# Optimization experiments

Hardware: AMD Instinct MI355X
Metric: run time of the kernel (lower is better)

## Reference

```python
import jax, jax.numpy as jnp
import numpy as np

VOCAB, VDIM, DDIM, BATCH = 50257, 300, 512, 16


def setup_inputs() -> dict:
    key = jax.random.key(0)
    k1, k2, k3, k4, k5 = jax.random.split(key, 5)
    return {
        "decoder_hidden": jax.random.normal(k1, (BATCH, DDIM), dtype=jnp.float32),
        "embedding_vocab": jax.random.normal(k2, (VOCAB, VDIM), dtype=jnp.float32),
        "W_dec": jax.random.normal(k3, (VDIM, DDIM), dtype=jnp.float32) * (1.0 / np.sqrt(DDIM)),
        "b_dec": jax.random.normal(k4, (VDIM,), dtype=jnp.float32) * 0.01,
        "W_full": jax.random.normal(k5, (VDIM,), dtype=jnp.float32) * (1.0 / np.sqrt(VDIM)),
        "b_full": jnp.zeros((), dtype=jnp.float32),
    }


def reference(decoder_hidden, embedding_vocab, W_dec, b_dec, W_full, b_full):
    # query: (B, vocab_dim) = decoder_att(decoder_hidden)
    query = decoder_hidden @ W_dec.T + b_dec
    # additive scores: relu(vocab + query) projected to scalar -> (B, V)
    hidden = jax.nn.relu(embedding_vocab[None, :, :] + query[:, None, :])  # (B, V, D)
    att = jnp.einsum("bvd,d->bv", hidden, W_full) + b_full
    alpha = jax.nn.softmax(att, axis=1)  # softmax over vocab
    # weighted sum of vocab embeddings: (B, vocab_dim)
    attention_weighted_encoding = jnp.einsum("bv,vd->bd", alpha, embedding_vocab)
    return attention_weighted_encoding, alpha
```

## Files before the change

### kernel.cpp

```cpp
#include <hip/hip_runtime.h>

constexpr int V  = 50257;
constexpr int D  = 300;
constexpr int KD = 512;
constexpr int B  = 16;

constexpr int ROWS = 32;
constexpr int NB_ATT = (V + ROWS - 1) / ROWS;
constexpr int NT = 5;
constexpr int NC  = 448;
constexpr int RPC = 113;

constexpr float NEG_HUGE = -1.0e30f;

constexpr size_t WS_QT   = 0;
constexpr size_t WS_STAT = 5120;
constexpr size_t WS_MS   = WS_STAT + (size_t)NB_ATT * 32;
constexpr size_t WS_PART = WS_MS + 32;
constexpr size_t WS_TMP  = WS_PART + (size_t)NC * 4800;

typedef float v2f __attribute__((ext_vector_type(2)));

struct f4 { float v[4]; };
__device__ __forceinline__ f4 ld4(const float* p) {
    float4 t = *(const float4*)p;
    return {t.x, t.y, t.z, t.w};
}

#define AS1 __attribute__((address_space(1)))
#define AS3 __attribute__((address_space(3)))
#define DPPF(x, CTRL) __int_as_float(__builtin_amdgcn_mov_dpp(__float_as_int(x), (CTRL), 0xF, 0xF, false))

__global__ void __launch_bounds__(256) k_query(
    const float* __restrict__ dh, const float* __restrict__ Wdec,
    const float* __restrict__ bdec, float* __restrict__ q_swz)
{
    int wid  = (blockIdx.x * 256 + threadIdx.x) >> 6;
    int lane = threadIdx.x & 63;
    if (wid >= 320 * 16) return;
    int d = wid >> 4, b = wid & 15;
    float s = 0.f;
    if (d < D) {
        const float* wrow = Wdec + (size_t)d * KD;
        const float* hrow = dh + (size_t)b * KD;
        for (int k = lane; k < KD; k += 64) s += wrow[k] * hrow[k];
        #pragma unroll
        for (int off = 32; off; off >>= 1) s += __shfl_down(s, off, 64);
        s += bdec[d];
    }
    if (lane == 0) {
        int P = (d >> 1) * 8 + ((((d & 1) << 2) | (b >> 2)) ^ ((d >> 2) & 7));
        q_swz[P * 4 + (b & 3)] = (d < D) ? s : 0.f;
    }
}

__global__ void __launch_bounds__(256) k_att(
    const float* __restrict__ E, const float* __restrict__ q_swz,
    const float* __restrict__ wf, const float* __restrict__ bf,
    float* __restrict__ att, float* __restrict__ blkstats)
{
    __shared__ __align__(16) float sq[5120];
    __shared__ __align__(16) float seE[9632];
    __shared__ float sms[768];

    const int t    = threadIdx.x;
    const int slot = t & 15;
    const int rg   = t >> 4;
    const int v0   = blockIdx.x * ROWS;

    #pragma unroll
    for (int k = 0; k < 5; ++k)
        __builtin_amdgcn_global_load_lds((const AS1 void*)(q_swz + k * 1024 + t * 4),
                                         (AS3 void*)(sq + k * 1024 + t * 4), 16, 0, 0);
    int nrow = V - v0; if (nrow > ROWS) nrow = ROWS;
    const int nflt = nrow * 300;
    const float* Eb = E + (size_t)v0 * 300;
    #pragma unroll
    for (int k = 0; k < 10; ++k) {
        int o = k * 1024 + t * 4;
        if (o < nflt)
            __builtin_amdgcn_global_load_lds((const AS1 void*)(Eb + o),
                                             (AS3 void*)(seE + o), 16, 0, 0);
    }
    if (t < 32) seE[9600 + t] = 0.f;

    f4 wreg[NT];
    #pragma unroll
    for (int k = 0; k < 4; ++k) wreg[k] = ld4(wf + k * 64 + slot * 4);
    if (slot < 11) wreg[4] = ld4(wf + 256 + slot * 4);
    else { wreg[4].v[0] = wreg[4].v[1] = wreg[4].v[2] = wreg[4].v[3] = 0.f; }
    #pragma unroll
    for (int i = 0; i < 4; ++i)
        if (256 + slot * 4 + i >= D && slot < 11) wreg[4].v[i] = 0.f;
    const float bfull = bf[0];

    int xq[2][4];
    #pragma unroll
    for (int i1 = 0; i1 < 2; ++i1)
        #pragma unroll
        for (int bq = 0; bq < 4; ++bq)
            xq[i1][bq] = slot * 64 + 4 * (((i1 << 2) | bq) ^ (slot & 7));

    v2f acc2[2][8];
    #pragma unroll
    for (int j = 0; j < 2; ++j)
        #pragma unroll
        for (int p = 0; p < 8; ++p) acc2[j][p] = (v2f){0.f, 0.f};

    __syncthreads();

    #pragma unroll
    for (int tt = 0; tt < NT; ++tt) {
        f4 e0 = ld4(seE + rg * 300 + tt * 64 + slot * 4);
        f4 e1 = ld4(seE + (rg + 16) * 300 + tt * 64 + slot * 4);
        const float* sqt = sq + tt * 1024;
        #pragma unroll
        for (int i = 0; i < 4; ++i) {
            float wi = wreg[tt].v[i];
            v2f w2 = {wi, wi};
            #pragma unroll
            for (int bq = 0; bq < 4; ++bq) {
                f4 qv = ld4(sqt + (i >> 1) * 32 + xq[i & 1][bq]);
                v2f qlo = {qv.v[0], qv.v[1]};
                v2f qhi = {qv.v[2], qv.v[3]};
                v2f z2  = {0.f, 0.f};
                v2f ea  = {e0.v[i], e0.v[i]};
                v2f lo0 = __builtin_elementwise_max(ea + qlo, z2);
                v2f hi0 = __builtin_elementwise_max(ea + qhi, z2);
                acc2[0][bq*2]   = __builtin_elementwise_fma(lo0, w2, acc2[0][bq*2]);
                acc2[0][bq*2+1] = __builtin_elementwise_fma(hi0, w2, acc2[0][bq*2+1]);
                v2f eb  = {e1.v[i], e1.v[i]};
                v2f lo1 = __builtin_elementwise_max(eb + qlo, z2);
                v2f hi1 = __builtin_elementwise_max(eb + qhi, z2);
                acc2[1][bq*2]   = __builtin_elementwise_fma(lo1, w2, acc2[1][bq*2]);
                acc2[1][bq*2+1] = __builtin_elementwise_fma(hi1, w2, acc2[1][bq*2+1]);
            }
        }
    }

    float acc[2][16];
    #pragma unroll
    for (int j = 0; j < 2; ++j)
        #pragma unroll
        for (int bq = 0; bq < 4; ++bq) {
            acc[j][bq*4+0] = acc2[j][bq*2][0];
            acc[j][bq*4+1] = acc2[j][bq*2][1];
            acc[j][bq*4+2] = acc2[j][bq*2+1][0];
            acc[j][bq*4+3] = acc2[j][bq*2+1][1];
        }

    #pragma unroll
    for (int j = 0; j < 2; ++j)
        #pragma unroll
        for (int b = 0; b < 16; ++b) {
            float x = acc[j][b];
            x += DPPF(x, 0xB1);
            x += DPPF(x, 0x4E);
            acc[j][b] = x;
        }
    const int c = slot & 3;
    float kept[2][4];
    #pragma unroll
    for (int j = 0; j < 2; ++j)
        #pragma unroll
        for (int kk = 0; kk < 4; ++kk) {
            float x = (c == 0) ? acc[j][kk]
                    : (c == 1) ? acc[j][4 + kk]
                    : (c == 2) ? acc[j][8 + kk]
                    :            acc[j][12 + kk];
            x += __shfl_xor(x, 4, 64);
            x += __shfl_xor(x, 8, 64);
            kept[j][kk] = x;
        }

    const int jown = (slot >> 2) & 1;
    const int dup  = slot >> 3;
    const int row  = v0 + rg + 16 * jown;
    const bool ok  = row < V;
    const int g    = rg + 16 * jown;
    #pragma unroll
    for (int kk2 = 0; kk2 < 2; ++kk2) {
        int b = 4 * c + (dup ? 2 : 0) + kk2;
        float x0 = jown ? kept[1][kk2]     : kept[0][kk2];
        float x1 = jown ? kept[1][2 + kk2] : kept[0][2 + kk2];
        float x  = (dup ? x1 : x0) + bfull;
        if (ok) att[(size_t)b * V + row] = x;
        sms[g * 16 + b] = ok ? x : NEG_HUGE;
    }
    __syncthreads();
    if (t < 128) {
        int b = t & 15, gq = t >> 4;
        float m = NEG_HUGE;
        #pragma unroll
        for (int u = 0; u < 4; ++u) m = fmaxf(m, sms[(gq * 4 + u) * 16 + b]);
        float s = 0.f;
        #pragma unroll
        for (int u = 0; u < 4; ++u) s += __expf(sms[(gq * 4 + u) * 16 + b] - m);
        sms[512 + gq * 16 + b] = m;
        sms[640 + gq * 16 + b] = s;
    }
    __syncthreads();
    if (t < 16) {
        float m = NEG_HUGE, s = 0.f;
        #pragma unroll
        for (int gq = 0; gq < 8; ++gq) {
            float mg = sms[512 + gq * 16 + t], sg = sms[640 + gq * 16 + t];
            float mn = fmaxf(m, mg);
            s = s * __expf(m - mn) + sg * __expf(mg - mn);
            m = mn;
        }
        blkstats[((size_t)blockIdx.x * 16 + t) * 2]     = m;
        blkstats[((size_t)blockIdx.x * 16 + t) * 2 + 1] = s;
    }
}

__global__ void __launch_bounds__(64) k_combine(
    const float* __restrict__ blkstats, float* __restrict__ MS)
{
    int b = blockIdx.x, lane = threadIdx.x;
    float m = NEG_HUGE;
    for (int cc = lane; cc < NB_ATT; cc += 64)
        m = fmaxf(m, blkstats[(size_t)(cc * 16 + b) * 2]);
    #pragma unroll
    for (int off = 32; off; off >>= 1) m = fmaxf(m, __shfl_xor(m, off, 64));
    float s = 0.f;
    for (int cc = lane; cc < NB_ATT; cc += 64)
        s += blkstats[(size_t)(cc * 16 + b) * 2 + 1] *
             __expf(blkstats[(size_t)(cc * 16 + b) * 2] - m);
    #pragma unroll
    for (int off = 32; off; off >>= 1) s += __shfl_xor(s, off, 64);
    if (lane == 0) { MS[b * 2] = m; MS[b * 2 + 1] = 1.f / s; }
}

__global__ void __launch_bounds__(320) k_awsum(
    const float* __restrict__ E, float* __restrict__ att,
    const float* __restrict__ MS, float* __restrict__ partials)
{
    __shared__ float sal[RPC * 16];
    int c = blockIdx.x, t = threadIdx.x;
    int v0 = c * RPC;
    int n = V - v0;
    if (n > RPC) n = RPC;
    if (n < 0) n = 0;

    for (int i = t; i < RPC * 16; i += 320) {
        int b = i / RPC, vv = i - b * RPC;
        float a = 0.f;
        if (vv < n) {
            float M = MS[b * 2], invS = MS[b * 2 + 1];
            size_t gi = (size_t)b * V + v0 + vv;
            a = __expf(att[gi] - M) * invS;
            att[gi] = a;
        }
        sal[vv * 16 + b] = a;
    }
    __syncthreads();

    if (t < D) {
        float acc[16];
        #pragma unroll
        for (int b = 0; b < 16; ++b) acc[b] = 0.f;
        #pragma unroll 8
        for (int vv = 0; vv < n; ++vv) {
            float e = E[(size_t)(v0 + vv) * D + t];
            const float* ap = sal + vv * 16;
            f4 a0 = ld4(ap), a1 = ld4(ap + 4), a2 = ld4(ap + 8), a3 = ld4(ap + 12);
            #pragma unroll
            for (int b = 0; b < 4; ++b) {
                acc[b]      = fmaf(a0.v[b], e, acc[b]);
                acc[b + 4]  = fmaf(a1.v[b], e, acc[b + 4]);
                acc[b + 8]  = fmaf(a2.v[b], e, acc[b + 8]);
                acc[b + 12] = fmaf(a3.v[b], e, acc[b + 12]);
            }
        }
        #pragma unroll
        for (int b = 0; b < 16; ++b)
            partials[(size_t)c * 4800 + b * D + t] = acc[b];
    }
}

__global__ void __launch_bounds__(256) k_red1(
    const float* __restrict__ partials, float* __restrict__ tmp)
{
    int o4 = blockIdx.x * 256 + threadIdx.x;
    if (o4 >= 1200) return;
    int y = blockIdx.y;
    float4 s = {0.f, 0.f, 0.f, 0.f};
    for (int c = y * 28; c < y * 28 + 28; ++c) {
        float4 p = *(const float4*)(partials + (size_t)c * 4800 + o4 * 4);
        s.x += p.x; s.y += p.y; s.z += p.z; s.w += p.w;
    }
    *(float4*)(tmp + (size_t)y * 4800 + o4 * 4) = s;
}

__global__ void __launch_bounds__(256) k_red2(
    const float* __restrict__ tmp, float* __restrict__ out)
{
    int o4 = blockIdx.x * 256 + threadIdx.x;
    if (o4 >= 1200) return;
    float4 s = {0.f, 0.f, 0.f, 0.f};
    #pragma unroll
    for (int y = 0; y < 16; ++y) {
        float4 p = *(const float4*)(tmp + (size_t)y * 4800 + o4 * 4);
        s.x += p.x; s.y += p.y; s.z += p.z; s.w += p.w;
    }
    *(float4*)(out + o4 * 4) = s;
}

extern "C" void kernel_launch(void* const* d_in, const int* in_sizes, int n_in,
                              void* d_out, int out_size, void* d_ws, size_t ws_size,
                              hipStream_t stream) {
    const float* dh   = (const float*)d_in[0];
    const float* E    = (const float*)d_in[1];
    const float* Wdec = (const float*)d_in[2];
    const float* bdec = (const float*)d_in[3];
    const float* wf   = (const float*)d_in[4];
    const float* bf   = (const float*)d_in[5];
    float* out = (float*)d_out;
    float* ws  = (float*)d_ws;

    float* q_swz = ws + WS_QT;
    float* stats = ws + WS_STAT;
    float* MS    = ws + WS_MS;
    float* part  = ws + WS_PART;
    float* tmp   = ws + WS_TMP;
    float* att   = out + 4800;

    k_query<<<(320 * 16) / 4, 256, 0, stream>>>(dh, Wdec, bdec, q_swz);
    k_att<<<NB_ATT, 256, 0, stream>>>(E, q_swz, wf, bf, att, stats);
    k_combine<<<B, 64, 0, stream>>>(stats, MS);
    k_awsum<<<NC, 320, 0, stream>>>(E, att, MS, part);
    k_red1<<<dim3(5, 16), 256, 0, stream>>>(part, tmp);
    k_red2<<<5, 256, 0, stream>>>(tmp, out);
}
```

Baseline: 74.37 us.

## Fuse attention scoring with online-softmax weighted sum over vocab tiles

```diff
diff --git a/kernel.cpp b/kernel.cpp
--- a/kernel.cpp
+++ b/kernel.cpp
@@ -5,19 +5,16 @@
 constexpr int KD = 512;
 constexpr int B  = 16;
 
-constexpr int ROWS = 32;
-constexpr int NB_ATT = (V + ROWS - 1) / ROWS;
-constexpr int NT = 5;
-constexpr int NC  = 448;
-constexpr int RPC = 113;
+constexpr int ROWS = 64;
+constexpr int NBLK = (V + ROWS - 1) / ROWS;
+constexpr int NSUB = NBLK * 2;
 
 constexpr float NEG_HUGE = -1.0e30f;
 
-constexpr size_t WS_QT   = 0;
-constexpr size_t WS_STAT = 5120;
-constexpr size_t WS_MS   = WS_STAT + (size_t)NB_ATT * 32;
-constexpr size_t WS_PART = WS_MS + 32;
-constexpr size_t WS_TMP  = WS_PART + (size_t)NC * 4800;
+constexpr size_t WS_QT    = 0;
+constexpr size_t WS_STAT  = 5120;
+constexpr size_t WS_SCALE = 55424;
+constexpr size_t WS_WPART = 80576;
 
 typedef float v2f __attribute__((ext_vector_type(2)));
 
@@ -54,14 +51,16 @@
     }
 }
 
-__global__ void __launch_bounds__(256) k_att(
+__global__ void __launch_bounds__(256, 2) k_att_pv(
     const float* __restrict__ E, const float* __restrict__ q_swz,
     const float* __restrict__ wf, const float* __restrict__ bf,
-    float* __restrict__ att, float* __restrict__ blkstats)
+    float* __restrict__ alpha, float* __restrict__ blkstats,
+    float* __restrict__ wpart)
 {
     __shared__ __align__(16) float sq[5120];
-    __shared__ __align__(16) float seE[9632];
-    __shared__ float sms[768];
+    __shared__ __align__(16) float seE[9600];
+    __shared__ float satt[512];
+    __shared__ float sm[16], sf[16], sold[16];
 
     const int t    = threadIdx.x;
     const int slot = t & 15;
@@ -72,19 +71,22 @@
     for (int k = 0; k < 5; ++k)
         __builtin_amdgcn_global_load_lds((const AS1 void*)(q_swz + k * 1024 + t * 4),
                                          (AS3 void*)(sq + k * 1024 + t * 4), 16, 0, 0);
-    int nrow = V - v0; if (nrow > ROWS) nrow = ROWS;
-    const int nflt = nrow * 300;
-    const float* Eb = E + (size_t)v0 * 300;
-    #pragma unroll
-    for (int k = 0; k < 10; ++k) {
-        int o = k * 1024 + t * 4;
-        if (o < nflt)
-            __builtin_amdgcn_global_load_lds((const AS1 void*)(Eb + o),
-                                             (AS3 void*)(seE + o), 16, 0, 0);
-    }
-    if (t < 32) seE[9600 + t] = 0.f;
-
-    f4 wreg[NT];
+    {
+        int nr = V - v0; if (nr > 32) nr = 32;
+        int nflt = nr * 300;
+        const float* Eb = E + (size_t)v0 * 300;
+        #pragma unroll
+        for (int k = 0; k < 10; ++k) {
+            int o = k * 1024 + t * 4;
+            if (o < nflt)
+                __builtin_amdgcn_global_load_lds((const AS1 void*)(Eb + o),
+                                                 (AS3 void*)(seE + o), 16, 0, 0);
+        }
+        for (int o = t * 4; o < 9600; o += 1024)
+            if (o >= nflt) *(float4*)(seE + o) = make_float4(0.f, 0.f, 0.f, 0.f);
+    }
+
+    f4 wreg[5];
     #pragma unroll
     for (int k = 0; k < 4; ++k) wreg[k] = ld4(wf + k * 64 + slot * 4);
     if (slot < 11) wreg[4] = ld4(wf + 256 + slot * 4);
@@ -101,210 +103,282 @@
         for (int bq = 0; bq < 4; ++bq)
             xq[i1][bq] = slot * 64 + 4 * (((i1 << 2) | bq) ^ (slot & 7));
 
-    v2f acc2[2][8];
-    #pragma unroll
-    for (int j = 0; j < 2; ++j)
-        #pragma unroll
-        for (int p = 0; p < 8; ++p) acc2[j][p] = (v2f){0.f, 0.f};
-
+    if (t < 16) sold[t] = NEG_HUGE;
+
+    const int dgrp = t & 15;
+    const int rh   = (t >> 4) & 1;
+    const int bp   = t >> 5;
+    const int b0   = bp * 2, b1 = bp * 2 + 1;
+    f4 pvA[5], pvB[5];
+    #pragma unroll
+    for (int k = 0; k < 5; ++k)
+        #pragma unroll
+        for (int c4 = 0; c4 < 4; ++c4) { pvA[k].v[c4] = 0.f; pvB[k].v[c4] = 0.f; }
+
+    asm volatile("s_waitcnt vmcnt(0)" ::: "memory");
     __syncthreads();
 
-    #pragma unroll
-    for (int tt = 0; tt < NT; ++tt) {
-        f4 e0 = ld4(seE + rg * 300 + tt * 64 + slot * 4);
-        f4 e1 = ld4(seE + (rg + 16) * 300 + tt * 64 + slot * 4);
-        const float* sqt = sq + tt * 1024;
-        #pragma unroll
-        for (int i = 0; i < 4; ++i) {
-            float wi = wreg[tt].v[i];
-            v2f w2 = {wi, wi};
-            #pragma unroll
-            for (int bq = 0; bq < 4; ++bq) {
-                f4 qv = ld4(sqt + (i >> 1) * 32 + xq[i & 1][bq]);
-                v2f qlo = {qv.v[0], qv.v[1]};
-                v2f qhi = {qv.v[2], qv.v[3]};
-                v2f z2  = {0.f, 0.f};
-                v2f ea  = {e0.v[i], e0.v[i]};
-                v2f lo0 = __builtin_elementwise_max(ea + qlo, z2);
-                v2f hi0 = __builtin_elementwise_max(ea + qhi, z2);
-                acc2[0][bq*2]   = __builtin_elementwise_fma(lo0, w2, acc2[0][bq*2]);
-                acc2[0][bq*2+1] = __builtin_elementwise_fma(hi0, w2, acc2[0][bq*2+1]);
-                v2f eb  = {e1.v[i], e1.v[i]};
-                v2f lo1 = __builtin_elementwise_max(eb + qlo, z2);
-                v2f hi1 = __builtin_elementwise_max(eb + qhi, z2);
-                acc2[1][bq*2]   = __builtin_elementwise_fma(lo1, w2, acc2[1][bq*2]);
-                acc2[1][bq*2+1] = __builtin_elementwise_fma(hi1, w2, acc2[1][bq*2+1]);
-            }
-        }
-    }
-
-    float acc[2][16];
-    #pragma unroll
-    for (int j = 0; j < 2; ++j)
-        #pragma unroll
-        for (int bq = 0; bq < 4; ++bq) {
-            acc[j][bq*4+0] = acc2[j][bq*2][0];
-            acc[j][bq*4+1] = acc2[j][bq*2][1];
-            acc[j][bq*4+2] = acc2[j][bq*2+1][0];
-            acc[j][bq*4+3] = acc2[j][bq*2+1][1];
-        }
-
-    #pragma unroll
-    for (int j = 0; j < 2; ++j)
-        #pragma unroll
-        for (int b = 0; b < 16; ++b) {
-            float x = acc[j][b];
-            x += DPPF(x, 0xB1);
-            x += DPPF(x, 0x4E);
-            acc[j][b] = x;
-        }
-    const int c = slot & 3;
-    float kept[2][4];
-    #pragma unroll
-    for (int j = 0; j < 2; ++j)
-        #pragma unroll
-        for (int kk = 0; kk < 4; ++kk) {
-            float x = (c == 0) ? acc[j][kk]
-                    : (c == 1) ? acc[j][4 + kk]
-                    : (c == 2) ? acc[j][8 + kk]
-                    :            acc[j][12 + kk];
-            x += __shfl_xor(x, 4, 64);
-            x += __shfl_xor(x, 8, 64);
-            kept[j][kk] = x;
-        }
-
+    const int c    = slot & 3;
     const int jown = (slot >> 2) & 1;
     const int dup  = slot >> 3;
-    const int row  = v0 + rg + 16 * jown;
-    const bool ok  = row < V;
-    const int g    = rg + 16 * jown;
-    #pragma unroll
-    for (int kk2 = 0; kk2 < 2; ++kk2) {
-        int b = 4 * c + (dup ? 2 : 0) + kk2;
-        float x0 = jown ? kept[1][kk2]     : kept[0][kk2];
-        float x1 = jown ? kept[1][2 + kk2] : kept[0][2 + kk2];
-        float x  = (dup ? x1 : x0) + bfull;
-        if (ok) att[(size_t)b * V + row] = x;
-        sms[g * 16 + b] = ok ? x : NEG_HUGE;
-    }
-    __syncthreads();
-    if (t < 128) {
-        int b = t & 15, gq = t >> 4;
-        float m = NEG_HUGE;
-        #pragma unroll
-        for (int u = 0; u < 4; ++u) m = fmaxf(m, sms[(gq * 4 + u) * 16 + b]);
-        float s = 0.f;
-        #pragma unroll
-        for (int u = 0; u < 4; ++u) s += __expf(sms[(gq * 4 + u) * 16 + b] - m);
-        sms[512 + gq * 16 + b] = m;
-        sms[640 + gq * 16 + b] = s;
-    }
-    __syncthreads();
-    if (t < 16) {
-        float m = NEG_HUGE, s = 0.f;
-        #pragma unroll
-        for (int gq = 0; gq < 8; ++gq) {
-            float mg = sms[512 + gq * 16 + t], sg = sms[640 + gq * 16 + t];
-            float mn = fmaxf(m, mg);
-            s = s * __expf(m - mn) + sg * __expf(mg - mn);
-            m = mn;
-        }
-        blkstats[((size_t)blockIdx.x * 16 + t) * 2]     = m;
-        blkstats[((size_t)blockIdx.x * 16 + t) * 2 + 1] = s;
+    const int lrow = rg + 16 * jown;
+
+    for (int sub = 0; sub < 2; ++sub) {
+        const int vs = v0 + sub * 32;
+
+        v2f acc2[2][8];
+        #pragma unroll
+        for (int j = 0; j < 2; ++j)
+            #pragma unroll
+            for (int p = 0; p < 8; ++p) acc2[j][p] = (v2f){0.f, 0.f};
+
+        #pragma unroll
+        for (int tt = 0; tt < 5; ++tt) {
+            f4 e0 = ld4(seE + rg * 300 + tt * 64 + slot * 4);
+            f4 e1 = ld4(seE + (rg + 16) * 300 + tt * 64 + slot * 4);
+            const float* sqt = sq + tt * 1024;
+            #pragma unroll
+            for (int i = 0; i < 4; ++i) {
+                float wi = wreg[tt].v[i];
+                v2f w2 = {wi, wi};
+                #pragma unroll
+                for (int bq = 0; bq < 4; ++bq) {
+                    f4 qv = ld4(sqt + (i >> 1) * 32 + xq[i & 1][bq]);
+                    v2f qlo = {qv.v[0], qv.v[1]};
+                    v2f qhi = {qv.v[2], qv.v[3]};
+                    v2f z2  = {0.f, 0.f};
+                    v2f ea  = {e0.v[i], e0.v[i]};
+                    v2f lo0 = __builtin_elementwise_max(ea + qlo, z2);
+                    v2f hi0 = __builtin_elementwise_max(ea + qhi, z2);
+                    acc2[0][bq*2]   = __builtin_elementwise_fma(lo0, w2, acc2[0][bq*2]);
+                    acc2[0][bq*2+1] = __builtin_elementwise_fma(hi0, w2, acc2[0][bq*2+1]);
+                    v2f eb  = {e1.v[i], e1.v[i]};
+                    v2f lo1 = __builtin_elementwise_max(eb + qlo, z2);
+                    v2f hi1 = __builtin_elementwise_max(eb + qhi, z2);
+                    acc2[1][bq*2]   = __builtin_elementwise_fma(lo1, w2, acc2[1][bq*2]);
+                    acc2[1][bq*2+1] = __builtin_elementwise_fma(hi1, w2, acc2[1][bq*2+1]);
+                }
+            }
+        }
+
+        float acc[2][16];
+        #pragma unroll
+        for (int j = 0; j < 2; ++j)
+            #pragma unroll
+            for (int bq = 0; bq < 4; ++bq) {
+                acc[j][bq*4+0] = acc2[j][bq*2][0];
+                acc[j][bq*4+1] = acc2[j][bq*2][1];
+                acc[j][bq*4+2] = acc2[j][bq*2+1][0];
+                acc[j][bq*4+3] = acc2[j][bq*2+1][1];
+            }
+
+        #pragma unroll
+        for (int j = 0; j < 2; ++j)
+            #pragma unroll
+            for (int b = 0; b < 16; ++b) {
+                float x = acc[j][b];
+                x += DPPF(x, 0xB1);
+                x += DPPF(x, 0x4E);
+                acc[j][b] = x;
+            }
+        float kept[2][4];
+        #pragma unroll
+        for (int j = 0; j < 2; ++j)
+            #pragma unroll
+            for (int kk = 0; kk < 4; ++kk) {
+                float x = (c == 0) ? acc[j][kk]
+                        : (c == 1) ? acc[j][4 + kk]
+                        : (c == 2) ? acc[j][8 + kk]
+                        :            acc[j][12 + kk];
+                x += __shfl_xor(x, 4, 64);
+                x += __shfl_xor(x, 8, 64);
+                kept[j][kk] = x;
+            }
+
+        const int grow = vs + lrow;
+        const bool ok  = grow < V;
+        #pragma unroll
+        for (int kk2 = 0; kk2 < 2; ++kk2) {
+            int b = 4 * c + (dup ? 2 : 0) + kk2;
+            float x0 = jown ? kept[1][kk2]     : kept[0][kk2];
+            float x1 = jown ? kept[1][2 + kk2] : kept[0][2 + kk2];
+            float x  = (dup ? x1 : x0) + bfull;
+            satt[lrow * 16 + b] = ok ? x : NEG_HUGE;
+        }
+        __syncthreads();
+
+        if (t < 16) {
+            float ms = NEG_HUGE;
+            #pragma unroll 4
+            for (int u = 0; u < 32; ++u) ms = fmaxf(ms, satt[u * 16 + t]);
+            float Mn = fmaxf(sold[t], ms);
+            float ss = 0.f;
+            #pragma unroll 4
+            for (int u = 0; u < 32; ++u) ss += __expf(satt[u * 16 + t] - Mn);
+            size_t sg = ((size_t)blockIdx.x * 2 + sub) * 16 + t;
+            blkstats[sg * 2]     = Mn;
+            blkstats[sg * 2 + 1] = ss;
+            sf[t] = __expf(sold[t] - Mn);
+            sm[t] = Mn;
+            sold[t] = Mn;
+        }
+        __syncthreads();
+
+        #pragma unroll
+        for (int kk2 = 0; kk2 < 2; ++kk2) {
+            int b = 4 * c + (dup ? 2 : 0) + kk2;
+            float p = __expf(satt[lrow * 16 + b] - sm[b]);
+            satt[lrow * 16 + b] = p;
+            if (ok) alpha[(size_t)b * V + grow] = p;
+        }
+        {
+            float fA = sf[b0], fB = sf[b1];
+            #pragma unroll
+            for (int k = 0; k < 5; ++k)
+                #pragma unroll
+                for (int c4 = 0; c4 < 4; ++c4) {
+                    pvA[k].v[c4] *= fA;
+                    pvB[k].v[c4] *= fB;
+                }
+        }
+        __syncthreads();
+
+        #pragma unroll 2
+        for (int r = 0; r < 16; ++r) {
+            int lr = rh * 16 + r;
+            float pA = satt[lr * 16 + b0];
+            float pB = satt[lr * 16 + b1];
+            const float* er = seE + lr * 300 + dgrp * 4;
+            #pragma unroll
+            for (int k = 0; k < 5; ++k) {
+                if (k < 4 || dgrp < 11) {
+                    f4 e = ld4(er + k * 64);
+                    #pragma unroll
+                    for (int c4 = 0; c4 < 4; ++c4) {
+                        pvA[k].v[c4] = fmaf(pA, e.v[c4], pvA[k].v[c4]);
+                        pvB[k].v[c4] = fmaf(pB, e.v[c4], pvB[k].v[c4]);
+                    }
+                }
+            }
+        }
+        __syncthreads();
+
+        if (sub == 0) {
+            int nr = V - (v0 + 32); if (nr > 32) nr = 32; if (nr < 0) nr = 0;
+            int nflt = nr * 300;
+            const float* Eb = E + (size_t)(v0 + 32) * 300;
+            #pragma unroll
+            for (int k = 0; k < 10; ++k) {
+                int o = k * 1024 + t * 4;
+                if (o < nflt)
+                    __builtin_amdgcn_global_load_lds((const AS1 void*)(Eb + o),
+                                                     (AS3 void*)(seE + o), 16, 0, 0);
+            }
+            for (int o = t * 4; o < 9600; o += 1024)
+                if (o >= nflt) *(float4*)(seE + o) = make_float4(0.f, 0.f, 0.f, 0.f);
+            asm volatile("s_waitcnt vmcnt(0)" ::: "memory");
+            __syncthreads();
+        }
+    }
+
+    #pragma unroll
+    for (int k = 0; k < 5; ++k)
+        #pragma unroll
+        for (int c4 = 0; c4 < 4; ++c4) {
+            pvA[k].v[c4] += __shfl_xor(pvA[k].v[c4], 16, 64);
+            pvB[k].v[c4] += __shfl_xor(pvB[k].v[c4], 16, 64);
+        }
+    {
+        int bsel = rh ? b1 : b0;
+        float* wp = wpart + (size_t)blockIdx.x * 4800 + bsel * 300;
+        #pragma unroll
+        for (int k = 0; k < 5; ++k) {
+            int d = k * 64 + dgrp * 4;
+            if (d < 300) {
+                float4 s;
+                if (rh) { s.x = pvB[k].v[0]; s.y = pvB[k].v[1]; s.z = pvB[k].v[2]; s.w = pvB[k].v[3]; }
+                else    { s.x = pvA[k].v[0]; s.y = pvA[k].v[1]; s.z = pvA[k].v[2]; s.w = pvA[k].v[3]; }
+                *(float4*)(wp + d) = s;
+            }
+        }
     }
 }
 
 __global__ void __launch_bounds__(64) k_combine(
-    const float* __restrict__ blkstats, float* __restrict__ MS)
+    const float* __restrict__ blkstats, float* __restrict__ scale)
 {
     int b = blockIdx.x, lane = threadIdx.x;
     float m = NEG_HUGE;
-    for (int cc = lane; cc < NB_ATT; cc += 64)
+    for (int cc = lane; cc < NSUB; cc += 64)
         m = fmaxf(m, blkstats[(size_t)(cc * 16 + b) * 2]);
     #pragma unroll
     for (int off = 32; off; off >>= 1) m = fmaxf(m, __shfl_xor(m, off, 64));
     float s = 0.f;
-    for (int cc = lane; cc < NB_ATT; cc += 64)
+    for (int cc = lane; cc < NSUB; cc += 64)
         s += blkstats[(size_t)(cc * 16 + b) * 2 + 1] *
              __expf(blkstats[(size_t)(cc * 16 + b) * 2] - m);
     #pragma unroll
     for (int off = 32; off; off >>= 1) s += __shfl_xor(s, off, 64);
-    if (lane == 0) { MS[b * 2] = m; MS[b * 2 + 1] = 1.f / s; }
-}
-
-__global__ void __launch_bounds__(320) k_awsum(
-    const float* __restrict__ E, float* __restrict__ att,
-    const float* __restrict__ MS, float* __restrict__ partials)
+    float invS = 1.f / s;
+    for (int cc = lane; cc < NSUB; cc += 64)
+        scale[(size_t)b * NSUB + cc] =
+            __expf(blkstats[(size_t)(cc * 16 + b) * 2] - m) * invS;
+}
+
+__global__ void __launch_bounds__(512) k_finish(
+    const float* __restrict__ wpart, const float* __restrict__ scale,
+    float* __restrict__ alpha, float* __restrict__ out)
 {
-    __shared__ float sal[RPC * 16];
-    int c = blockIdx.x, t = threadIdx.x;
-    int v0 = c * RPC;
-    int n = V - v0;
-    if (n > RPC) n = RPC;
-    if (n < 0) n = 0;
-
-    for (int i = t; i < RPC * 16; i += 320) {
-        int b = i / RPC, vv = i - b * RPC;
-        float a = 0.f;
-        if (vv < n) {
-            float M = MS[b * 2], invS = MS[b * 2 + 1];
-            size_t gi = (size_t)b * V + v0 + vv;
-            a = __expf(att[gi] - M) * invS;
-            att[gi] = a;
-        }
-        sal[vv * 16 + b] = a;
-    }
-    __syncthreads();
-
-    if (t < D) {
-        float acc[16];
-        #pragma unroll
-        for (int b = 0; b < 16; ++b) acc[b] = 0.f;
-        #pragma unroll 8
-        for (int vv = 0; vv < n; ++vv) {
-            float e = E[(size_t)(v0 + vv) * D + t];
-            const float* ap = sal + vv * 16;
-            f4 a0 = ld4(ap), a1 = ld4(ap + 4), a2 = ld4(ap + 8), a3 = ld4(ap + 12);
-            #pragma unroll
-            for (int b = 0; b < 4; ++b) {
-                acc[b]      = fmaf(a0.v[b], e, acc[b]);
-                acc[b + 4]  = fmaf(a1.v[b], e, acc[b + 4]);
-                acc[b + 8]  = fmaf(a2.v[b], e, acc[b + 8]);
-                acc[b + 12] = fmaf(a3.v[b], e, acc[b + 12]);
-            }
-        }
-        #pragma unroll
-        for (int b = 0; b < 16; ++b)
-            partials[(size_t)c * 4800 + b * D + t] = acc[b];
-    }
-}
-
-__global__ void __launch_bounds__(256) k_red1(
-    const float* __restrict__ partials, float* __restrict__ tmp)
-{
-    int o4 = blockIdx.x * 256 + threadIdx.x;
-    if (o4 >= 1200) return;
-    int y = blockIdx.y;
-    float4 s = {0.f, 0.f, 0.f, 0.f};
-    for (int c = y * 28; c < y * 28 + 28; ++c) {
-        float4 p = *(const float4*)(partials + (size_t)c * 4800 + o4 * 4);
-        s.x += p.x; s.y += p.y; s.z += p.z; s.w += p.w;
-    }
-    *(float4*)(tmp + (size_t)y * 4800 + o4 * 4) = s;
-}
-
-__global__ void __launch_bounds__(256) k_red2(
-    const float* __restrict__ tmp, float* __restrict__ out)
-{
-    int o4 = blockIdx.x * 256 + threadIdx.x;
-    if (o4 >= 1200) return;
-    float4 s = {0.f, 0.f, 0.f, 0.f};
-    #pragma unroll
-    for (int y = 0; y < 16; ++y) {
-        float4 p = *(const float4*)(tmp + (size_t)y * 4800 + o4 * 4);
-        s.x += p.x; s.y += p.y; s.z += p.z; s.w += p.w;
-    }
-    *(float4*)(out + o4 * 4) = s;
+    __shared__ float red[512];
+    int bi = blockIdx.x, t = threadIdx.x;
+    if (bi < 80) {
+        int b = bi / 5, dq = bi % 5;
+        int dd = t & 63, blane = t >> 6;
+        int d = dq * 64 + dd;
+        float acc = 0.f;
+        if (d < 300) {
+            const float* sc = scale + (size_t)b * NSUB;
+            int w0 = blane * 99, w1 = w0 + 99;
+            if (w1 > NBLK) w1 = NBLK;
+            int w = w0;
+            for (; w + 8 <= w1; w += 8) {
+                #pragma unroll
+                for (int u = 0; u < 8; ++u)
+                    acc = fmaf(wpart[(size_t)(w + u) * 4800 + b * 300 + d],
+                               sc[2 * (w + u) + 1], acc);
+            }
+            for (; w < w1; ++w)
+                acc = fmaf(wpart[(size_t)w * 4800 + b * 300 + d],
+                           sc[2 * w + 1], acc);
+        }
+        red[blane * 64 + dd] = acc;
+        __syncthreads();
+        if (t < 64) {
+            float s = 0.f;
+            #pragma unroll
+            for (int l = 0; l < 8; ++l) s += red[l * 64 + t];
+            int d2 = dq * 64 + t;
+            if (d2 < 300) out[b * 300 + d2] = s;
+        }
+    } else {
+        int bid2 = bi - 80;
+        int b = bid2 / 5, seg = bid2 % 5;
+        const float* sc = scale + (size_t)b * NSUB;
+        float* al = alpha + (size_t)b * V;
+        #pragma unroll
+        for (int i = 0; i < 5; ++i) {
+            int v = seg * 10240 + i * 2048 + t * 4;
+            if (v + 4 <= V) {
+                float4 a = *(const float4*)(al + v);
+                float s = sc[v >> 5];
+                a.x *= s; a.y *= s; a.z *= s; a.w *= s;
+                *(float4*)(al + v) = a;
+            } else {
+                for (int vv = v; vv < V && vv < v + 4; ++vv)
+                    al[vv] *= sc[vv >> 5];
+            }
+        }
+    }
 }
 
 extern "C" void kernel_launch(void* const* d_in, const int* in_sizes, int n_in,
@@ -321,15 +395,12 @@
 
     float* q_swz = ws + WS_QT;
     float* stats = ws + WS_STAT;
-    float* MS    = ws + WS_MS;
-    float* part  = ws + WS_PART;
-    float* tmp   = ws + WS_TMP;
-    float* att   = out + 4800;
+    float* scale = ws + WS_SCALE;
+    float* wpart = ws + WS_WPART;
+    float* alpha = out + 4800;
 
     k_query<<<(320 * 16) / 4, 256, 0, stream>>>(dh, Wdec, bdec, q_swz);
-    k_att<<<NB_ATT, 256, 0, stream>>>(E, q_swz, wf, bf, att, stats);
-    k_combine<<<B, 64, 0, stream>>>(stats, MS);
-    k_awsum<<<NC, 320, 0, stream>>>(E, att, MS, part);
-    k_red1<<<dim3(5, 16), 256, 0, stream>>>(part, tmp);
-    k_red2<<<5, 256, 0, stream>>>(tmp, out);
-}
+    k_att_pv<<<NBLK, 256, 0, stream>>>(E, q_swz, wf, bf, alpha, stats, wpart);
+    k_combine<<<B, 64, 0, stream>>>(stats, scale);
+    k_finish<<<160, 512, 0, stream>>>(wpart, scale, alpha, out);
+}
```

Measured after the change: 88.75 us. 1.19x slower.

## Merge two-stage reduction into one kernel and prefetch query tiles in k_att

Applied to the files above, without the earlier changes.

```diff
diff --git a/kernel.cpp b/kernel.cpp
--- a/kernel.cpp
+++ b/kernel.cpp
@@ -17,7 +17,6 @@
 constexpr size_t WS_STAT = 5120;
 constexpr size_t WS_MS   = WS_STAT + (size_t)NB_ATT * 32;
 constexpr size_t WS_PART = WS_MS + 32;
-constexpr size_t WS_TMP  = WS_PART + (size_t)NC * 4800;
 
 typedef float v2f __attribute__((ext_vector_type(2)));
 
@@ -54,7 +53,7 @@
     }
 }
 
-__global__ void __launch_bounds__(256) k_att(
+__global__ void __launch_bounds__(256, 2) k_att(
     const float* __restrict__ E, const float* __restrict__ q_swz,
     const float* __restrict__ wf, const float* __restrict__ bf,
     float* __restrict__ att, float* __restrict__ blkstats)
@@ -83,6 +82,8 @@
                                              (AS3 void*)(seE + o), 16, 0, 0);
     }
     if (t < 32) seE[9600 + t] = 0.f;
+    for (int o = t * 4; o < 9600; o += 1024)
+        if (o >= nflt) *(float4*)(seE + o) = make_float4(0.f, 0.f, 0.f, 0.f);
 
     f4 wreg[NT];
     #pragma unroll
@@ -114,15 +115,20 @@
         f4 e0 = ld4(seE + rg * 300 + tt * 64 + slot * 4);
         f4 e1 = ld4(seE + (rg + 16) * 300 + tt * 64 + slot * 4);
         const float* sqt = sq + tt * 1024;
+        f4 qv[4][4];
+        #pragma unroll
+        for (int i = 0; i < 4; ++i)
+            #pragma unroll
+            for (int bq = 0; bq < 4; ++bq)
+                qv[i][bq] = ld4(sqt + (i >> 1) * 32 + xq[i & 1][bq]);
         #pragma unroll
         for (int i = 0; i < 4; ++i) {
             float wi = wreg[tt].v[i];
             v2f w2 = {wi, wi};
             #pragma unroll
             for (int bq = 0; bq < 4; ++bq) {
-                f4 qv = ld4(sqt + (i >> 1) * 32 + xq[i & 1][bq]);
-                v2f qlo = {qv.v[0], qv.v[1]};
-                v2f qhi = {qv.v[2], qv.v[3]};
+                v2f qlo = {qv[i][bq].v[0], qv[i][bq].v[1]};
+                v2f qhi = {qv[i][bq].v[2], qv[i][bq].v[3]};
                 v2f z2  = {0.f, 0.f};
                 v2f ea  = {e0.v[i], e0.v[i]};
                 v2f lo0 = __builtin_elementwise_max(ea + qlo, z2);
@@ -279,30 +285,18 @@
     }
 }
 
-__global__ void __launch_bounds__(256) k_red1(
-    const float* __restrict__ partials, float* __restrict__ tmp)
-{
-    int o4 = blockIdx.x * 256 + threadIdx.x;
-    if (o4 >= 1200) return;
-    int y = blockIdx.y;
-    float4 s = {0.f, 0.f, 0.f, 0.f};
-    for (int c = y * 28; c < y * 28 + 28; ++c) {
-        float4 p = *(const float4*)(partials + (size_t)c * 4800 + o4 * 4);
-        s.x += p.x; s.y += p.y; s.z += p.z; s.w += p.w;
-    }
-    *(float4*)(tmp + (size_t)y * 4800 + o4 * 4) = s;
-}
-
-__global__ void __launch_bounds__(256) k_red2(
-    const float* __restrict__ tmp, float* __restrict__ out)
+__global__ void __launch_bounds__(256) k_red(
+    const float* __restrict__ partials, float* __restrict__ out)
 {
     int o4 = blockIdx.x * 256 + threadIdx.x;
     if (o4 >= 1200) return;
     float4 s = {0.f, 0.f, 0.f, 0.f};
-    #pragma unroll
-    for (int y = 0; y < 16; ++y) {
-        float4 p = *(const float4*)(tmp + (size_t)y * 4800 + o4 * 4);
-        s.x += p.x; s.y += p.y; s.z += p.z; s.w += p.w;
+    for (int c = 0; c < NC; c += 8) {
+        #pragma unroll
+        for (int u = 0; u < 8; ++u) {
+            float4 p = *(const float4*)(partials + (size_t)(c + u) * 4800 + o4 * 4);
+            s.x += p.x; s.y += p.y; s.z += p.z; s.w += p.w;
+        }
     }
     *(float4*)(out + o4 * 4) = s;
 }
@@ -323,13 +317,11 @@
     float* stats = ws + WS_STAT;
     float* MS    = ws + WS_MS;
     float* part  = ws + WS_PART;
-    float* tmp   = ws + WS_TMP;
     float* att   = out + 4800;
 
     k_query<<<(320 * 16) / 4, 256, 0, stream>>>(dh, Wdec, bdec, q_swz);
     k_att<<<NB_ATT, 256, 0, stream>>>(E, q_swz, wf, bf, att, stats);
     k_combine<<<B, 64, 0, stream>>>(stats, MS);
     k_awsum<<<NC, 320, 0, stream>>>(E, att, MS, part);
-    k_red1<<<dim3(5, 16), 256, 0, stream>>>(part, tmp);
-    k_red2<<<5, 256, 0, stream>>>(tmp, out);
-}
+    k_red<<<5, 256, 0, stream>>>(part, out);
+}
```

Result: slower. 91.96 us (+23.7%).
